# Kernel optimization log

Measured on AMD Instinct MI355X. Metric: run time of the kernel, lower is better.

## Reference

```python
import jax, jax.numpy as jnp
import numpy as np

D = 1e-6
B, N, E, K = 128, 512, 512, 256


def _lower_median_abs(x, axis):
    # torch.median returns the LOWER of the two middle values for even counts
    n = x.shape[axis]
    s = jnp.sort(jnp.abs(x), axis=axis)
    return jnp.take(s, (n - 1) // 2, axis=axis)


def _bounds_from_cauchy(head, errors, k):
    # errors: (B, E, *head.shape[1:]); E divisible by k in this config
    b, e = errors.shape[0], errors.shape[1]
    tail = errors.shape[2:]
    chunks = errors.reshape(b, e // k, k, *tail)
    l1 = _lower_median_abs(chunks, axis=2).sum(axis=1)
    return head - l1, head + l1


def _relaxed_exp(h, errs, noise, lb, ub):
    is_tight = ub == lb
    lam_s = (jnp.exp(ub) - jnp.exp(lb)) / (ub - lb + D)
    lam = jnp.minimum(lam_s, jnp.exp(lb + 1.0 - 0.1))
    ub0 = jnp.where(lam > lam_s, jnp.exp(lb) - lam * lb, jnp.exp(ub) - lam * ub)
    mu = 0.5 * (lam * (1.0 - jnp.log(lam)) + ub0)
    delta = 0.5 * (ub0 - lam * (1.0 - jnp.log(lam)))
    lam = jnp.where(is_tight, 0.0, lam)
    mu = jnp.where(is_tight, jnp.exp(ub), mu)
    delta = jnp.where(is_tight, 0.0, delta)
    new_head = h * lam + mu
    new_errs = jnp.concatenate([errs * lam[:, None], delta[:, None] * noise], axis=1)
    return new_head, new_errs


def _relaxed_log(h, errs, noise, lb, ub):
    is_tight = ub == lb
    lam_s = (jnp.log(ub) - jnp.log(lb + D)) / (ub - lb + D)
    lam = lam_s
    lb0 = jnp.where(lam < lam_s, jnp.log(ub) - ub * lam, jnp.log(lb + D) - lb * lam)
    mu = 0.5 * (-jnp.log(lam) - 1.0 + lb0)
    delta = 0.5 * (-jnp.log(lam) - 1.0 - lb0)
    lam = jnp.where(is_tight, 0.0, lam)
    mu = jnp.where(is_tight, jnp.log(ub), mu)
    delta = jnp.where(is_tight, 0.0, delta)
    new_head = h * lam + mu
    new_errs = jnp.concatenate([errs * lam[:, None], delta[:, None] * noise], axis=1)
    return new_head, new_errs


def setup_inputs() -> dict:
    key = jax.random.key(0)
    k1, k2, k3, k4 = jax.random.split(key, 4)
    curr_head = jax.random.normal(k1, (B, N), dtype=jnp.float32)
    # small error magnitudes keep exp/log relaxation bounds valid (lb of log stage > 0)
    curr_errors = 1e-3 * jax.random.normal(k2, (B * E, N), dtype=jnp.float32)
    cauchy_exp = jax.random.cauchy(k3, (B, K, N), dtype=jnp.float32)
    cauchy_log = jax.random.cauchy(k4, (B, K), dtype=jnp.float32)
    return {"curr_head": curr_head, "curr_errors": curr_errors,
            "cauchy_exp": cauchy_exp, "cauchy_log": cauchy_log, "k": K}


def reference(curr_head, curr_errors, cauchy_exp, cauchy_log, k):
    b, n = curr_head.shape
    max_head = jax.lax.stop_gradient(jnp.max(curr_head, axis=1, keepdims=True))  # (B,1)
    temp_head = curr_head - max_head                         # (B,N)
    errs = curr_errors.reshape(b, -1, n)                     # (B,E,N)
    lb, ub = _bounds_from_cauchy(temp_head, errs, k)
    exp_head, exp_errs = _relaxed_exp(temp_head, errs, cauchy_exp, lb, ub)  # (B,N),(B,E+K,N)
    exp_head = exp_head.sum(axis=1)                          # (B,)
    exp_errs = exp_errs.sum(axis=2)                          # (B,E+K)
    lb2, ub2 = _bounds_from_cauchy(exp_head, exp_errs, k)
    ls_head, ls_errs = _relaxed_log(exp_head, exp_errs, cauchy_log, lb2, ub2)  # (B,),(B,E+2K)
    ls_head = ls_head + max_head[:, 0]
    return ls_head, ls_errs.reshape(-1)
```

## Files before the change

kernel.cpp:

```cpp
#include <hip/hip_runtime.h>
#include <cstdint>
#include <cstddef>

#define BB 128
#define NN 512
#define EE 512
#define KK 256

__device__ __forceinline__ float wave_reduce_max(float v) {
#pragma unroll
  for (int off = 32; off >= 1; off >>= 1) v = fmaxf(v, __shfl_xor(v, off, 64));
  return v;
}
__device__ __forceinline__ float wave_reduce_sum(float v) {
#pragma unroll
  for (int off = 32; off >= 1; off >>= 1) v += __shfl_xor(v, off, 64);
  return v;
}

__device__ __forceinline__ float wave_median256(float a0, float a1, float a2, float a3) {
  float m = fmaxf(fmaxf(a0, a1), fmaxf(a2, a3));
  m = wave_reduce_max(m);
  float hi = __uint_as_float(__float_as_uint(m) + 1u);
  float lo = 0.f;
  float pivot = hi;
  bool found = false;
  for (int it = 0; it < 40; ++it) {
    pivot = 0.5f * (lo + hi);
    int cnt = __popcll(__ballot(a0 < pivot)) + __popcll(__ballot(a1 < pivot)) +
              __popcll(__ballot(a2 < pivot)) + __popcll(__ballot(a3 < pivot));
    if (cnt == 128) { found = true; break; }
    if (cnt < 128) lo = pivot; else hi = pivot;
  }
  float p = found ? pivot : hi;
  float s0 = (a0 < p) ? a0 : 0.f;
  float s1 = (a1 < p) ? a1 : 0.f;
  float s2 = (a2 < p) ? a2 : 0.f;
  float s3 = (a3 < p) ? a3 : 0.f;
  return wave_reduce_max(fmaxf(fmaxf(s0, s1), fmaxf(s2, s3)));
}

__global__ void kmax(const float* __restrict__ head, float* __restrict__ ws_max) {
  int b = blockIdx.x;
  int lane = threadIdx.x;
  const float* h = head + (size_t)b * NN;
  float m = -INFINITY;
#pragma unroll
  for (int i = 0; i < NN / 64; ++i) m = fmaxf(m, h[lane + 64 * i]);
  m = wave_reduce_max(m);
  if (lane == 0) ws_max[b] = m;
}

__global__ __launch_bounds__(256) void kstage1(
    const float* __restrict__ head, const float* __restrict__ errs,
    const float* __restrict__ ws_max, float* __restrict__ ws_lam,
    float* __restrict__ ws_delta, float* __restrict__ ws_ht) {
  __shared__ float tile[256 * 34];
  __shared__ float l1buf[32];
  const int b = blockIdx.x >> 4;
  const int n0 = (blockIdx.x & 15) * 32;
  const int tid = threadIdx.x;
  const int wave = tid >> 6, lane = tid & 63;
  if (tid < 32) l1buf[tid] = 0.f;
  __syncthreads();
  const int tr = tid >> 3, tc = (tid & 7) * 4;
  for (int c = 0; c < 2; ++c) {
    const float* src = errs + ((size_t)(b * EE + c * 256)) * NN + n0;
#pragma unroll
    for (int i = 0; i < 8; ++i) {
      int row = i * 32 + tr;
      float4 v = *(const float4*)(src + (size_t)row * NN + tc);
      float* dst = &tile[row * 34 + tc];
      *(float2*)dst = make_float2(v.x, v.y);
      *(float2*)(dst + 2) = make_float2(v.z, v.w);
    }
    __syncthreads();
#pragma unroll 1
    for (int jj = 0; jj < 8; ++jj) {
      int j = wave * 8 + jj;
      float a0 = fabsf(tile[lane * 34 + j]);
      float a1 = fabsf(tile[(lane + 64) * 34 + j]);
      float a2 = fabsf(tile[(lane + 128) * 34 + j]);
      float a3 = fabsf(tile[(lane + 192) * 34 + j]);
      float med = wave_median256(a0, a1, a2, a3);
      if (lane == 0) l1buf[j] += med;
    }
    __syncthreads();
  }
  if (tid < 32) {
    int n = n0 + tid;
    float l1 = l1buf[tid];
    float th = head[(size_t)b * NN + n] - ws_max[b];
    float lb = th - l1, ub = th + l1;
    float lam, mu;
    float delta;
    if (ub == lb) {
      lam = 0.f; mu = expf(ub); delta = 0.f;
    } else {
      float elb = expf(lb), eub = expf(ub);
      float lam_s = (eub - elb) / (ub - lb + 1e-6f);
      lam = fminf(lam_s, expf(lb + 0.9f));
      float ub0 = (lam > lam_s) ? (elb - lam * lb) : (eub - lam * ub);
      float t = lam * (1.f - logf(lam));
      mu = 0.5f * (t + ub0);
      delta = 0.5f * (ub0 - t);
    }
    size_t o = (size_t)b * NN + n;
    ws_lam[o] = lam;
    ws_delta[o] = delta;
    ws_ht[o] = th * lam + mu;
  }
}

__global__ __launch_bounds__(256) void kstage2(
    const float* __restrict__ errs, const float* __restrict__ cexp,
    const float* __restrict__ ws_lam, const float* __restrict__ ws_delta,
    float* __restrict__ ws_ee) {
  const int blk = blockIdx.x;
  const int b = blk / 12, part = blk % 12;
  const int wave = threadIdx.x >> 6, lane = threadIdx.x & 63;
  const bool is_err = part < 8;
  const float* wsrc = (is_err ? ws_lam : ws_delta) + (size_t)b * NN;
  float4 wa = *(const float4*)(wsrc + 4 * lane);
  float4 wb = *(const float4*)(wsrc + 256 + 4 * lane);
  const int r0 = (is_err ? part : part - 8) * 64 + wave * 16;
  const float* base = is_err ? (errs + (size_t)b * EE * NN) : (cexp + (size_t)b * KK * NN);
  float* out = ws_ee + (size_t)b * 768 + (is_err ? 0 : EE);
#pragma unroll 1
  for (int i = 0; i < 16; ++i) {
    int r = r0 + i;
    const float* rp = base + (size_t)r * NN;
    float4 x = *(const float4*)(rp + 4 * lane);
    float4 y = *(const float4*)(rp + 256 + 4 * lane);
    float s = x.x * wa.x + x.y * wa.y + x.z * wa.z + x.w * wa.w +
              y.x * wb.x + y.y * wb.y + y.z * wb.z + y.w * wb.w;
    s = wave_reduce_sum(s);
    if (lane == 0) out[r] = s;
  }
}

__global__ __launch_bounds__(256) void kstage3(
    const float* __restrict__ clog, const float* __restrict__ ws_max,
    const float* __restrict__ ws_ht, const float* __restrict__ ws_ee,
    float* __restrict__ out) {
  __shared__ float red[4];
  __shared__ float meds[3];
  __shared__ float sc[2];
  const int b = blockIdx.x;
  const int tid = threadIdx.x, wave = tid >> 6, lane = tid & 63;
  float s = ws_ht[(size_t)b * NN + tid] + ws_ht[(size_t)b * NN + 256 + tid];
  s = wave_reduce_sum(s);
  if (lane == 0) red[wave] = s;
  const float* eb = ws_ee + (size_t)b * 768;
  if (wave < 3) {
    const float* p = eb + wave * 256;
    float a0 = fabsf(p[lane]), a1 = fabsf(p[lane + 64]);
    float a2 = fabsf(p[lane + 128]), a3 = fabsf(p[lane + 192]);
    float med = wave_median256(a0, a1, a2, a3);
    if (lane == 0) meds[wave] = med;
  }
  __syncthreads();
  if (tid == 0) {
    float eh = red[0] + red[1] + red[2] + red[3];
    float l1 = meds[0] + meds[1] + meds[2];
    float lb = eh - l1, ub = eh + l1;
    float lam, mu, delta;
    if (ub == lb) {
      lam = 0.f; mu = logf(ub); delta = 0.f;
    } else {
      float llb = logf(lb + 1e-6f);
      float lam_s = (logf(ub) - llb) / (ub - lb + 1e-6f);
      lam = lam_s;
      float lb0 = llb - lb * lam;
      float t = -logf(lam) - 1.f;
      mu = 0.5f * (t + lb0);
      delta = 0.5f * (t - lb0);
    }
    sc[0] = lam; sc[1] = delta;
    out[b] = eh * lam + mu + ws_max[b];
  }
  __syncthreads();
  float lam = sc[0], delta = sc[1];
  float* ob = out + BB + (size_t)b * 1024;
  ob[tid] = eb[tid] * lam;
  ob[tid + 256] = eb[tid + 256] * lam;
  ob[tid + 512] = eb[tid + 512] * lam;
  ob[tid + 768] = delta * clog[(size_t)b * KK + tid];
}

extern "C" void kernel_launch(void* const* d_in, const int* in_sizes, int n_in,
                              void* d_out, int out_size, void* d_ws, size_t ws_size,
                              hipStream_t stream) {
  const float* head = (const float*)d_in[0];
  const float* errs = (const float*)d_in[1];
  const float* cexp = (const float*)d_in[2];
  const float* clog = (const float*)d_in[3];
  float* out = (float*)d_out;

  float* ws = (float*)d_ws;
  float* ws_max = ws;
  float* ws_lam = ws + 128;
  float* ws_delta = ws_lam + BB * NN;
  float* ws_ht = ws_delta + BB * NN;
  float* ws_ee = ws_ht + BB * NN;

  hipLaunchKernelGGL(kmax, dim3(BB), dim3(64), 0, stream, head, ws_max);
  hipLaunchKernelGGL(kstage1, dim3(BB * 16), dim3(256), 0, stream,
                     head, errs, ws_max, ws_lam, ws_delta, ws_ht);
  hipLaunchKernelGGL(kstage2, dim3(BB * 12), dim3(256), 0, stream,
                     errs, cexp, ws_lam, ws_delta, ws_ee);
  hipLaunchKernelGGL(kstage3, dim3(BB), dim3(256), 0, stream,
                     clog, ws_max, ws_ht, ws_ee, out);
}
```

Baseline: 271.8 us.

## Fuse max, median bounds and error projection to read errors once

Merges the row-max kernel and the exp-bound kernel into one kernel that holds a 512x16 error tile in shared memory. The same tile is then reused to compute the lam-weighted error sums, so the separate pass that re-read the whole error tensor from global memory is gone. Each tile produces per-block partial sums, and the head sums are also written as partials; the final kernel reduces both and recomputes the row max. The aim is to cut one full pass over the large error tensor and one kernel launch. In exchange it adds an 8 MB partial-sum buffer and uses a larger shared-memory tile per block, which may limit occupancy.

```diff
diff --git a/kernel.cpp b/kernel.cpp
--- a/kernel.cpp
+++ b/kernel.cpp
@@ -6,6 +6,7 @@
 #define NN 512
 #define EE 512
 #define KK 256
+#define STR 17
 
 __device__ __forceinline__ float wave_reduce_max(float v) {
 #pragma unroll
@@ -40,60 +41,56 @@
   return wave_reduce_max(fmaxf(fmaxf(s0, s1), fmaxf(s2, s3)));
 }
 
-__global__ void kmax(const float* __restrict__ head, float* __restrict__ ws_max) {
-  int b = blockIdx.x;
-  int lane = threadIdx.x;
-  const float* h = head + (size_t)b * NN;
-  float m = -INFINITY;
-#pragma unroll
-  for (int i = 0; i < NN / 64; ++i) m = fmaxf(m, h[lane + 64 * i]);
+__global__ __launch_bounds__(256, 4) void kfused(
+    const float* __restrict__ head, const float* __restrict__ errs,
+    float* __restrict__ ws_delta, float* __restrict__ ws_htpart,
+    float* __restrict__ ws_epart) {
+  __shared__ float tile[512 * STR];
+  __shared__ float medbuf[32];
+  __shared__ float lambuf[16];
+  __shared__ float redm[4];
+  const int blk = blockIdx.x;
+  const int b = blk >> 5, g = blk & 31;
+  const int n0 = g * 16;
+  const int tid = threadIdx.x, wave = tid >> 6, lane = tid & 63;
+
+  float m = fmaxf(head[(size_t)b * NN + tid], head[(size_t)b * NN + 256 + tid]);
   m = wave_reduce_max(m);
-  if (lane == 0) ws_max[b] = m;
-}
-
-__global__ __launch_bounds__(256) void kstage1(
-    const float* __restrict__ head, const float* __restrict__ errs,
-    const float* __restrict__ ws_max, float* __restrict__ ws_lam,
-    float* __restrict__ ws_delta, float* __restrict__ ws_ht) {
-  __shared__ float tile[256 * 34];
-  __shared__ float l1buf[32];
-  const int b = blockIdx.x >> 4;
-  const int n0 = (blockIdx.x & 15) * 32;
-  const int tid = threadIdx.x;
-  const int wave = tid >> 6, lane = tid & 63;
-  if (tid < 32) l1buf[tid] = 0.f;
-  __syncthreads();
-  const int tr = tid >> 3, tc = (tid & 7) * 4;
-  for (int c = 0; c < 2; ++c) {
-    const float* src = errs + ((size_t)(b * EE + c * 256)) * NN + n0;
-#pragma unroll
-    for (int i = 0; i < 8; ++i) {
-      int row = i * 32 + tr;
-      float4 v = *(const float4*)(src + (size_t)row * NN + tc);
-      float* dst = &tile[row * 34 + tc];
-      *(float2*)dst = make_float2(v.x, v.y);
-      *(float2*)(dst + 2) = make_float2(v.z, v.w);
-    }
-    __syncthreads();
+  if (lane == 0) redm[wave] = m;
+
+  const int tr = tid >> 2, tc = (tid & 3) * 4;
+  const float* src = errs + (size_t)b * EE * NN + n0 + tc;
+#pragma unroll
+  for (int i = 0; i < 8; ++i) {
+    int row = i * 64 + tr;
+    float4 v = *(const float4*)(src + (size_t)row * NN);
+    float* dst = &tile[row * STR + tc];
+    dst[0] = v.x; dst[1] = v.y; dst[2] = v.z; dst[3] = v.w;
+  }
+  __syncthreads();
+  float hmax = fmaxf(fmaxf(redm[0], redm[1]), fmaxf(redm[2], redm[3]));
+
 #pragma unroll 1
-    for (int jj = 0; jj < 8; ++jj) {
-      int j = wave * 8 + jj;
-      float a0 = fabsf(tile[lane * 34 + j]);
-      float a1 = fabsf(tile[(lane + 64) * 34 + j]);
-      float a2 = fabsf(tile[(lane + 128) * 34 + j]);
-      float a3 = fabsf(tile[(lane + 192) * 34 + j]);
-      float med = wave_median256(a0, a1, a2, a3);
-      if (lane == 0) l1buf[j] += med;
-    }
-    __syncthreads();
-  }
-  if (tid < 32) {
+  for (int jj = 0; jj < 8; ++jj) {
+    int p = wave * 8 + jj;
+    int col = p & 15;
+    int rb = (p >> 4) * 256;
+    float a0 = fabsf(tile[(rb + lane) * STR + col]);
+    float a1 = fabsf(tile[(rb + lane + 64) * STR + col]);
+    float a2 = fabsf(tile[(rb + lane + 128) * STR + col]);
+    float a3 = fabsf(tile[(rb + lane + 192) * STR + col]);
+    float med = wave_median256(a0, a1, a2, a3);
+    if (lane == 0) medbuf[p] = med;
+  }
+  __syncthreads();
+
+  float htp = 0.f;
+  if (tid < 16) {
     int n = n0 + tid;
-    float l1 = l1buf[tid];
-    float th = head[(size_t)b * NN + n] - ws_max[b];
+    float l1 = medbuf[tid] + medbuf[16 + tid];
+    float th = head[(size_t)b * NN + n] - hmax;
     float lb = th - l1, ub = th + l1;
-    float lam, mu;
-    float delta;
+    float lam, mu, delta;
     if (ub == lb) {
       lam = 0.f; mu = expf(ub); delta = 0.f;
     } else {
@@ -105,27 +102,40 @@
       mu = 0.5f * (t + ub0);
       delta = 0.5f * (ub0 - t);
     }
-    size_t o = (size_t)b * NN + n;
-    ws_lam[o] = lam;
-    ws_delta[o] = delta;
-    ws_ht[o] = th * lam + mu;
-  }
-}
-
-__global__ __launch_bounds__(256) void kstage2(
-    const float* __restrict__ errs, const float* __restrict__ cexp,
-    const float* __restrict__ ws_lam, const float* __restrict__ ws_delta,
-    float* __restrict__ ws_ee) {
+    lambuf[tid] = lam;
+    ws_delta[(size_t)b * NN + n] = delta;
+    htp = th * lam + mu;
+  }
+  if (wave == 0) {
+    float s = wave_reduce_sum(htp);
+    if (lane == 0) ws_htpart[b * 32 + g] = s;
+  }
+  __syncthreads();
+
+  float s0 = 0.f, s1 = 0.f;
+#pragma unroll
+  for (int j = 0; j < 16; ++j) {
+    float w = lambuf[j];
+    s0 = fmaf(tile[tid * STR + j], w, s0);
+    s1 = fmaf(tile[(tid + 256) * STR + j], w, s1);
+  }
+  float* op = ws_epart + ((size_t)(b * 32 + g)) * 512;
+  op[tid] = s0;
+  op[tid + 256] = s1;
+}
+
+__global__ __launch_bounds__(256) void kcexp(
+    const float* __restrict__ cexp, const float* __restrict__ ws_delta,
+    float* __restrict__ ws_ee2) {
   const int blk = blockIdx.x;
-  const int b = blk / 12, part = blk % 12;
+  const int b = blk >> 2, part = blk & 3;
   const int wave = threadIdx.x >> 6, lane = threadIdx.x & 63;
-  const bool is_err = part < 8;
-  const float* wsrc = (is_err ? ws_lam : ws_delta) + (size_t)b * NN;
+  const float* wsrc = ws_delta + (size_t)b * NN;
   float4 wa = *(const float4*)(wsrc + 4 * lane);
   float4 wb = *(const float4*)(wsrc + 256 + 4 * lane);
-  const int r0 = (is_err ? part : part - 8) * 64 + wave * 16;
-  const float* base = is_err ? (errs + (size_t)b * EE * NN) : (cexp + (size_t)b * KK * NN);
-  float* out = ws_ee + (size_t)b * 768 + (is_err ? 0 : EE);
+  const int r0 = part * 64 + wave * 16;
+  const float* base = cexp + (size_t)b * KK * NN;
+  float* out = ws_ee2 + (size_t)b * KK;
 #pragma unroll 1
   for (int i = 0; i < 16; ++i) {
     int r = r0 + i;
@@ -140,28 +150,49 @@
 }
 
 __global__ __launch_bounds__(256) void kstage3(
-    const float* __restrict__ clog, const float* __restrict__ ws_max,
-    const float* __restrict__ ws_ht, const float* __restrict__ ws_ee,
-    float* __restrict__ out) {
-  __shared__ float red[4];
+    const float* __restrict__ head, const float* __restrict__ clog,
+    const float* __restrict__ ws_htpart, const float* __restrict__ ws_epart,
+    const float* __restrict__ ws_ee2, float* __restrict__ out) {
+  __shared__ float eb[768];
+  __shared__ float redm[4];
   __shared__ float meds[3];
   __shared__ float sc[2];
+  __shared__ float ehsh;
   const int b = blockIdx.x;
   const int tid = threadIdx.x, wave = tid >> 6, lane = tid & 63;
-  float s = ws_ht[(size_t)b * NN + tid] + ws_ht[(size_t)b * NN + 256 + tid];
-  s = wave_reduce_sum(s);
-  if (lane == 0) red[wave] = s;
-  const float* eb = ws_ee + (size_t)b * 768;
+
+  float m = fmaxf(head[(size_t)b * NN + tid], head[(size_t)b * NN + 256 + tid]);
+  m = wave_reduce_max(m);
+  if (lane == 0) redm[wave] = m;
+
+  float acc0 = 0.f, acc1 = 0.f;
+  const float* pp = ws_epart + (size_t)b * 32 * 512;
+#pragma unroll
+  for (int g = 0; g < 32; ++g) {
+    acc0 += pp[g * 512 + tid];
+    acc1 += pp[g * 512 + 256 + tid];
+  }
+  eb[tid] = acc0;
+  eb[tid + 256] = acc1;
+  eb[512 + tid >= 768 ? 0 : 512 + tid] = ws_ee2[(size_t)b * KK + tid];
+  __syncthreads();
+
   if (wave < 3) {
     const float* p = eb + wave * 256;
     float a0 = fabsf(p[lane]), a1 = fabsf(p[lane + 64]);
     float a2 = fabsf(p[lane + 128]), a3 = fabsf(p[lane + 192]);
     float med = wave_median256(a0, a1, a2, a3);
     if (lane == 0) meds[wave] = med;
-  }
-  __syncthreads();
+  } else {
+    float v = (lane < 32) ? ws_htpart[b * 32 + lane] : 0.f;
+    v = wave_reduce_sum(v);
+    if (lane == 0) ehsh = v;
+  }
+  __syncthreads();
+
   if (tid == 0) {
-    float eh = red[0] + red[1] + red[2] + red[3];
+    float hmax = fmaxf(fmaxf(redm[0], redm[1]), fmaxf(redm[2], redm[3]));
+    float eh = ehsh;
     float l1 = meds[0] + meds[1] + meds[2];
     float lb = eh - l1, ub = eh + l1;
     float lam, mu, delta;
@@ -177,7 +208,7 @@
       delta = 0.5f * (t - lb0);
     }
     sc[0] = lam; sc[1] = delta;
-    out[b] = eh * lam + mu + ws_max[b];
+    out[b] = eh * lam + mu + hmax;
   }
   __syncthreads();
   float lam = sc[0], delta = sc[1];
@@ -198,17 +229,15 @@
   float* out = (float*)d_out;
 
   float* ws = (float*)d_ws;
-  float* ws_max = ws;
-  float* ws_lam = ws + 128;
-  float* ws_delta = ws_lam + BB * NN;
-  float* ws_ht = ws_delta + BB * NN;
-  float* ws_ee = ws_ht + BB * NN;
-
-  hipLaunchKernelGGL(kmax, dim3(BB), dim3(64), 0, stream, head, ws_max);
-  hipLaunchKernelGGL(kstage1, dim3(BB * 16), dim3(256), 0, stream,
-                     head, errs, ws_max, ws_lam, ws_delta, ws_ht);
-  hipLaunchKernelGGL(kstage2, dim3(BB * 12), dim3(256), 0, stream,
-                     errs, cexp, ws_lam, ws_delta, ws_ee);
+  float* ws_delta = ws;
+  float* ws_htpart = ws_delta + BB * NN;
+  float* ws_ee2 = ws_htpart + BB * 32;
+  float* ws_epart = ws_ee2 + BB * KK;
+
+  hipLaunchKernelGGL(kfused, dim3(BB * 32), dim3(256), 0, stream,
+                     head, errs, ws_delta, ws_htpart, ws_epart);
+  hipLaunchKernelGGL(kcexp, dim3(BB * 4), dim3(256), 0, stream,
+                     cexp, ws_delta, ws_ee2);
   hipLaunchKernelGGL(kstage3, dim3(BB), dim3(256), 0, stream,
-                     clog, ws_max, ws_ht, ws_ee, out);
-}
+                     head, clog, ws_htpart, ws_epart, ws_ee2, out);
+}
```

Result: no change. 274.8 us (+1.1%).
